# Performance work log

Measured on AMD Instinct MI355X. Metric: run time of the kernel, lower is better.

## Reference

```python
import jax, jax.numpy as jnp
import numpy as np

NEG_SLOPE = 0.2

def gat_conv(x, src, dst, W, a_src, a_dst, b, n_nodes):
    # x: [N, Fin] -> h: [N, Fout]; edges (src->dst) incl. self-loops
    h = x @ W                                   # [N, Fout]
    as_ = h @ a_src                             # [N] per-node source score
    ad_ = h @ a_dst                             # [N] per-node dest score
    e = jax.nn.leaky_relu(as_[src] + ad_[dst], NEG_SLOPE)   # [E]
    # segment softmax over edges sharing the same destination
    e_max = jax.ops.segment_max(e, dst, num_segments=n_nodes)
    e_exp = jnp.exp(e - e_max[dst])
    e_sum = jax.ops.segment_sum(e_exp, dst, num_segments=n_nodes)
    alpha = e_exp / (e_sum[dst] + 1e-16)        # [E]
    out = jax.ops.segment_sum(alpha[:, None] * h[src], dst, num_segments=n_nodes)
    return out + b

def setup_inputs() -> dict:
    key = jax.random.key(0)
    ks = jax.random.split(key, 12)
    N, E, Fin, H = 100000, 3200000, 128, 32
    def g(k, shape, scale):
        return jax.random.normal(k, shape, dtype=jnp.float32) * scale
    return {
        "x": g(ks[0], (N, Fin), 1.0),
        "edge_index": jax.random.randint(ks[1], (2, E), 0, N, dtype=jnp.int32),
        "W1": g(ks[2], (Fin, H), 1.0 / np.sqrt(Fin)),
        "att_src1": g(ks[3], (H,), 1.0 / np.sqrt(H)),
        "att_dst1": g(ks[4], (H,), 1.0 / np.sqrt(H)),
        "b1": jnp.zeros((H,), jnp.float32),
        "W2": g(ks[5], (H, H), 1.0 / np.sqrt(H)),
        "att_src2": g(ks[6], (H,), 1.0 / np.sqrt(H)),
        "att_dst2": g(ks[7], (H,), 1.0 / np.sqrt(H)),
        "b2": jnp.zeros((H,), jnp.float32),
        "Wf": g(ks[8], (H, H), 1.0 / np.sqrt(H)),
        "bf": jnp.zeros((H,), jnp.float32),
    }

def reference(x, edge_index, W1, att_src1, att_dst1, b1, W2, att_src2, att_dst2, b2, Wf, bf):
    n_nodes = x.shape[0]
    loops = jnp.arange(n_nodes, dtype=edge_index.dtype)
    src = jnp.concatenate([edge_index[0], loops])  # add_self_loops=True (PyG default)
    dst = jnp.concatenate([edge_index[1], loops])
    h = jax.nn.relu(gat_conv(x, src, dst, W1, att_src1, att_dst1, b1, n_nodes))
    h = jax.nn.relu(gat_conv(h, src, dst, W2, att_src2, att_dst2, b2, n_nodes))
    return h @ Wf + bf
```

## Files before the change

### kernel.cpp

```cpp
#include <hip/hip_runtime.h>

#define NEG_SLOPE 0.2f
#define BK_SH 8
#define BK_SZ 256
#define MAXBUCK 512
#define EPB 8192

typedef _Float16 half8 __attribute__((ext_vector_type(8)));
typedef float f32x4 __attribute__((ext_vector_type(4)));

__global__ __launch_bounds__(256) void k_castW(const float* __restrict__ W,
                                               _Float16* __restrict__ Wt,
                                               int K) {
  for (int i = threadIdx.x; i < K * 32; i += 256) {
    int k = i >> 5, f = i & 31;
    Wt[f * K + k] = (_Float16)W[i];
  }
}

__global__ __launch_bounds__(256) void k_feat1(
    const float* __restrict__ x, const _Float16* __restrict__ Wt,
    const float* __restrict__ a_src, const float* __restrict__ a_dst,
    _Float16* __restrict__ Hh, float* __restrict__ as_, float* __restrict__ ad_,
    int N) {
  int w = threadIdx.x >> 6;
  int lane = threadIdx.x & 63;
  int base = (blockIdx.x * 4 + w) * 16;
  if (base >= N) return;
  int row16 = lane & 15;
  int kg = lane >> 4;
  f32x4 acc0 = {0.f, 0.f, 0.f, 0.f};
  f32x4 acc1 = {0.f, 0.f, 0.f, 0.f};
  const float* xr = x + (size_t)(base + row16) * 128 + kg * 8;
#pragma unroll
  for (int kt = 0; kt < 4; ++kt) {
    float4 u0 = *reinterpret_cast<const float4*>(xr + kt * 32);
    float4 u1 = *reinterpret_cast<const float4*>(xr + kt * 32 + 4);
    half8 a;
    a[0] = (_Float16)u0.x; a[1] = (_Float16)u0.y;
    a[2] = (_Float16)u0.z; a[3] = (_Float16)u0.w;
    a[4] = (_Float16)u1.x; a[5] = (_Float16)u1.y;
    a[6] = (_Float16)u1.z; a[7] = (_Float16)u1.w;
    half8 b0 = *reinterpret_cast<const half8*>(Wt + (size_t)row16 * 128 +
                                               kt * 32 + kg * 8);
    half8 b1 = *reinterpret_cast<const half8*>(Wt + (size_t)(16 + row16) * 128 +
                                               kt * 32 + kg * 8);
    acc0 = __builtin_amdgcn_mfma_f32_16x16x32_f16(a, b0, acc0, 0, 0, 0);
    acc1 = __builtin_amdgcn_mfma_f32_16x16x32_f16(a, b1, acc1, 0, 0, 0);
  }
  float aS0 = a_src[row16], aS1 = a_src[16 + row16];
  float aD0 = a_dst[row16], aD1 = a_dst[16 + row16];
  float tS[4], tD[4];
#pragma unroll
  for (int r = 0; r < 4; ++r) {
    int row = base + kg * 4 + r;
    Hh[(size_t)row * 32 + row16] = (_Float16)acc0[r];
    Hh[(size_t)row * 32 + 16 + row16] = (_Float16)acc1[r];
    tS[r] = acc0[r] * aS0 + acc1[r] * aS1;
    tD[r] = acc0[r] * aD0 + acc1[r] * aD1;
  }
#pragma unroll
  for (int off = 1; off <= 8; off <<= 1) {
#pragma unroll
    for (int r = 0; r < 4; ++r) {
      tS[r] += __shfl_xor(tS[r], off, 64);
      tD[r] += __shfl_xor(tD[r], off, 64);
    }
  }
  if (row16 == 0) {
#pragma unroll
    for (int r = 0; r < 4; ++r) {
      as_[base + kg * 4 + r] = tS[r];
      ad_[base + kg * 4 + r] = tD[r];
    }
  }
}

__global__ __launch_bounds__(256) void k_feat2(
    const _Float16* __restrict__ Bh, const _Float16* __restrict__ Wt,
    const float* __restrict__ a_src, const float* __restrict__ a_dst,
    _Float16* __restrict__ Hh, float* __restrict__ as_, float* __restrict__ ad_,
    int N) {
  int w = threadIdx.x >> 6;
  int lane = threadIdx.x & 63;
  int base = (blockIdx.x * 4 + w) * 16;
  if (base >= N) return;
  int row16 = lane & 15;
  int kg = lane >> 4;
  half8 a = *reinterpret_cast<const half8*>(Bh + (size_t)(base + row16) * 32 +
                                            kg * 8);
  half8 b0 =
      *reinterpret_cast<const half8*>(Wt + (size_t)row16 * 32 + kg * 8);
  half8 b1 =
      *reinterpret_cast<const half8*>(Wt + (size_t)(16 + row16) * 32 + kg * 8);
  f32x4 acc0 = {0.f, 0.f, 0.f, 0.f};
  f32x4 acc1 = {0.f, 0.f, 0.f, 0.f};
  acc0 = __builtin_amdgcn_mfma_f32_16x16x32_f16(a, b0, acc0, 0, 0, 0);
  acc1 = __builtin_amdgcn_mfma_f32_16x16x32_f16(a, b1, acc1, 0, 0, 0);
  float aS0 = a_src[row16], aS1 = a_src[16 + row16];
  float aD0 = a_dst[row16], aD1 = a_dst[16 + row16];
  float tS[4], tD[4];
#pragma unroll
  for (int r = 0; r < 4; ++r) {
    int row = base + kg * 4 + r;
    Hh[(size_t)row * 32 + row16] = (_Float16)acc0[r];
    Hh[(size_t)row * 32 + 16 + row16] = (_Float16)acc1[r];
    tS[r] = acc0[r] * aS0 + acc1[r] * aS1;
    tD[r] = acc0[r] * aD0 + acc1[r] * aD1;
  }
#pragma unroll
  for (int off = 1; off <= 8; off <<= 1) {
#pragma unroll
    for (int r = 0; r < 4; ++r) {
      tS[r] += __shfl_xor(tS[r], off, 64);
      tD[r] += __shfl_xor(tD[r], off, 64);
    }
  }
  if (row16 == 0) {
#pragma unroll
    for (int r = 0; r < 4; ++r) {
      as_[base + kg * 4 + r] = tS[r];
      ad_[base + kg * 4 + r] = tD[r];
    }
  }
}

__global__ __launch_bounds__(256) void k_zero(int* __restrict__ p, int n) {
  int i = blockIdx.x * 256 + threadIdx.x;
  if (i < n) p[i] = 0;
}

__global__ __launch_bounds__(256) void k_bhist(const int* __restrict__ ei,
                                               int E, int* __restrict__ bcnt,
                                               int* __restrict__ hmatT,
                                               int nb, int nbuck) {
  __shared__ int h[MAXBUCK];
  for (int i = threadIdx.x; i < nbuck; i += 256) h[i] = 0;
  __syncthreads();
  long base = (long)blockIdx.x * EPB;
#pragma unroll 4
  for (int i = 0; i < EPB / 256; ++i) {
    long e = base + i * 256 + threadIdx.x;
    if (e < E) atomicAdd(&h[ei[E + e] >> BK_SH], 1);
  }
  __syncthreads();
  for (int i = threadIdx.x; i < nbuck; i += 256) {
    hmatT[(size_t)i * nb + blockIdx.x] = h[i];
    if (h[i]) atomicAdd(&bcnt[i], h[i]);
  }
}

__global__ __launch_bounds__(1024) void k_scan(const int* __restrict__ bcnt,
                                               int* __restrict__ boff,
                                               int* __restrict__ ptr, int nbuck,
                                               int N, int E) {
  __shared__ int s[1024];
  int t = threadIdx.x;
  int v = (t < nbuck) ? bcnt[t] : 0;
  s[t] = v;
  __syncthreads();
  for (int off = 1; off < 1024; off <<= 1) {
    int x = (t >= off) ? s[t - off] : 0;
    __syncthreads();
    s[t] += x;
    __syncthreads();
  }
  if (t < nbuck) boff[t] = s[t] - v;
  if (t == 0) {
    boff[nbuck] = E;
    ptr[N] = E;
  }
}

__global__ __launch_bounds__(256) void k_colscan(const int* __restrict__ hmatT,
                                                 int* __restrict__ lbgT,
                                                 const int* __restrict__ boff,
                                                 int nb, int nbuck) {
  int wid = (blockIdx.x * 256 + threadIdx.x) >> 6;
  int lane = threadIdx.x & 63;
  if (wid >= nbuck) return;
  const int* row = hmatT + (size_t)wid * nb;
  int* orow = lbgT + (size_t)wid * nb;
  int base = boff[wid];
  for (int c = 0; c < nb; c += 64) {
    int v = (c + lane < nb) ? row[c + lane] : 0;
    int s = v;
#pragma unroll
    for (int off = 1; off < 64; off <<= 1) {
      int x = __shfl_up(s, off, 64);
      if (lane >= off) s += x;
    }
    if (c + lane < nb) orow[c + lane] = base + s - v;
    base += __shfl(s, 63, 64);
  }
}

__global__ __launch_bounds__(256) void k_binA(
    const int* __restrict__ ei, int E, const int* __restrict__ hmatT,
    const int* __restrict__ lbgT, unsigned* __restrict__ packed, int nb,
    int nbuck) {
  __shared__ int h[MAXBUCK];
  __shared__ int lbase[MAXBUCK];
  __shared__ int lb[MAXBUCK];
  __shared__ int cur[MAXBUCK];
  __shared__ int psum[256];
  __shared__ unsigned rec[EPB];
  __shared__ unsigned char bkt[EPB];
  int t = threadIdx.x;
  for (int i = t; i < MAXBUCK; i += 256) {
    h[i] = (i < nbuck) ? hmatT[(size_t)i * nb + blockIdx.x] : 0;
    lbase[i] = (i < nbuck) ? lbgT[(size_t)i * nb + blockIdx.x] : 0;
  }
  __syncthreads();
  long base = (long)blockIdx.x * EPB;
  int cnt = (int)((E - base) < EPB ? (E - base) : EPB);
  int a0 = h[2 * t], a1 = h[2 * t + 1];
  psum[t] = a0 + a1;
  __syncthreads();
  for (int off = 1; off < 256; off <<= 1) {
    int x = (t >= off) ? psum[t - off] : 0;
    __syncthreads();
    psum[t] += x;
    __syncthreads();
  }
  int pex = psum[t] - (a0 + a1);
  lb[2 * t] = pex;
  lb[2 * t + 1] = pex + a0;
  cur[2 * t] = pex;
  cur[2 * t + 1] = pex + a0;
  __syncthreads();
#pragma unroll 4
  for (int i = 0; i < EPB / 256; ++i) {
    int e = i * 256 + t;
    if (e < cnt) {
      int s = ei[base + e], d = ei[E + base + e];
      int b = d >> BK_SH;
      int pos = atomicAdd(&cur[b], 1);
      rec[pos] = ((unsigned)s << 8) | (unsigned)(d & (BK_SZ - 1));
      bkt[pos] = (unsigned char)b;
    }
  }
  __syncthreads();
  for (int i = t; i < cnt; i += 256) {
    int b0 = bkt[i];
    int b = (i >= lb[b0] && i < cur[b0]) ? b0 : b0 + 256;
    packed[(size_t)lbase[b] + (i - lb[b])] = rec[i];
  }
}

__global__ __launch_bounds__(256) void k_binB(const unsigned* __restrict__ packed,
                                              const int* __restrict__ boff,
                                              int* __restrict__ ptr,
                                              int* __restrict__ srcs, int N) {
  int b = blockIdx.x;
  int beg = boff[b], end = boff[b + 1];
  int t = threadIdx.x;
  __shared__ int lcnt[BK_SZ];
  __shared__ int sc[BK_SZ];
  __shared__ int lcur[BK_SZ];
  lcnt[t] = 0;
  __syncthreads();
  for (int i = beg + t; i < end; i += 256)
    atomicAdd(&lcnt[packed[i] & (BK_SZ - 1)], 1);
  __syncthreads();
  int v = lcnt[t];
  sc[t] = v;
  __syncthreads();
  for (int off = 1; off < 256; off <<= 1) {
    int x = (t >= off) ? sc[t - off] : 0;
    __syncthreads();
    sc[t] += x;
    __syncthreads();
  }
  int excl = sc[t] - v;
  int node = (b << BK_SH) + t;
  if (node < N) ptr[node] = beg + excl;
  lcur[t] = excl;
  __syncthreads();
  for (int i = beg + t; i < end; i += 256) {
    unsigned p = packed[i];
    int slot = atomicAdd(&lcur[p & (BK_SZ - 1)], 1);
    srcs[(size_t)beg + slot] = (int)(p >> 8);
  }
}

template <int FINAL>
__global__ __launch_bounds__(256) void k_gatherT(
    const int* __restrict__ ptr, const int* __restrict__ srcs,
    const _Float16* __restrict__ Hh, const float* __restrict__ as_,
    const float* __restrict__ ad_, const float* __restrict__ b,
    const float* __restrict__ Wf, const float* __restrict__ bf,
    void* __restrict__ OUTv, int N) {
  __shared__ float sWf[32 * 32];
  __shared__ float sO[8][33];
  if (FINAL) {
    for (int i = threadIdx.x; i < 32 * 32; i += 256) sWf[i] = Wf[i];
  }
  int g = threadIdx.x >> 5;
  int lane = threadIdx.x & 31;
  int sub = lane >> 2;
  int q = lane & 3;
  int d = blockIdx.x * 8 + g;
  int dc = d < N ? d : N - 1;
  float ad_d = ad_[dc];
  float acc[8] = {0.f, 0.f, 0.f, 0.f, 0.f, 0.f, 0.f, 0.f};
  float sumw = 0.f;
  int beg = ptr[dc], end = ptr[dc + 1];
  bool v0 = sub < end - beg;
  int sid0 = v0 ? srcs[beg + sub] : dc;
  float sa0 = as_[sid0];
  half8 hv0 = *reinterpret_cast<const half8*>(Hh + (size_t)sid0 * 32 + q * 8);
  bool v1 = sub < end - (beg + 8);
  int sid1 = v1 ? srcs[beg + 8 + sub] : dc;
  float sa1 = as_[sid1];
  half8 hv1 = *reinterpret_cast<const half8*>(Hh + (size_t)sid1 * 32 + q * 8);
  int nb8 = (end - beg + 7) >> 3;
  int j = beg;
#pragma unroll 2
  for (int it = 0; it < nb8; ++it) {
    int jn = j + 16;
    bool v2 = sub < end - jn;
    int sid2 = v2 ? srcs[jn + sub] : dc;
    float sa2 = as_[sid2];
    half8 hv2 = *reinterpret_cast<const half8*>(Hh + (size_t)sid2 * 32 + q * 8);
    float sc2 = sa0 + ad_d;
    float el = sc2 > 0.f ? sc2 : NEG_SLOPE * sc2;
    float w = v0 ? __expf(el) : 0.f;
#pragma unroll
    for (int i = 0; i < 8; ++i) acc[i] += w * (float)hv0[i];
    sumw += w;
    j = j + 8;
    v0 = v1; sid0 = sid1; sa0 = sa1; hv0 = hv1;
    v1 = v2; sid1 = sid2; sa1 = sa2; hv1 = hv2;
  }
#pragma unroll
  for (int off = 4; off <= 16; off <<= 1) {
#pragma unroll
    for (int i = 0; i < 8; ++i) acc[i] += __shfl_xor(acc[i], off, 32);
    sumw += __shfl_xor(sumw, off, 32);
  }
  if (sub == 0) {
    float s0 = as_[dc] + ad_d;
    float e0 = s0 > 0.f ? s0 : NEG_SLOPE * s0;
    float w0 = __expf(e0);
    half8 hs = *reinterpret_cast<const half8*>(Hh + (size_t)dc * 32 + q * 8);
#pragma unroll
    for (int i = 0; i < 8; ++i) acc[i] += w0 * (float)hs[i];
    sumw += w0;
    float inv = 1.f / (sumw + 1e-16f);
    if (FINAL) {
#pragma unroll
      for (int i = 0; i < 8; ++i)
        sO[g][q * 8 + i] = fmaxf(acc[i] * inv + b[q * 8 + i], 0.f);
    } else if (d < N) {
      half8 o;
#pragma unroll
      for (int i = 0; i < 8; ++i)
        o[i] = (_Float16)fmaxf(acc[i] * inv + b[q * 8 + i], 0.f);
      *reinterpret_cast<half8*>((_Float16*)OUTv + (size_t)d * 32 + q * 8) = o;
    }
  }
  if (FINAL) {
    __syncthreads();
    float accf = bf[lane];
#pragma unroll
    for (int k = 0; k < 32; ++k) accf += sO[g][k] * sWf[k * 32 + lane];
    if (d < N) ((float*)OUTv)[(size_t)d * 32 + lane] = accf;
  }
}

extern "C" void kernel_launch(void* const* d_in, const int* in_sizes, int n_in,
                              void* d_out, int out_size, void* d_ws,
                              size_t ws_size, hipStream_t stream) {
  const float* x = (const float*)d_in[0];
  const int* ei = (const int*)d_in[1];
  const float* W1 = (const float*)d_in[2];
  const float* as1 = (const float*)d_in[3];
  const float* ad1 = (const float*)d_in[4];
  const float* b1 = (const float*)d_in[5];
  const float* W2 = (const float*)d_in[6];
  const float* as2 = (const float*)d_in[7];
  const float* ad2 = (const float*)d_in[8];
  const float* b2 = (const float*)d_in[9];
  const float* Wf = (const float*)d_in[10];
  const float* bf = (const float*)d_in[11];
  float* out = (float*)d_out;

  const int H = in_sizes[3];
  const int FIN = in_sizes[2] / H;
  const int N = in_sizes[0] / FIN;
  const int E = in_sizes[1] / 2;
  const int nbuck = (N + BK_SZ - 1) >> BK_SH;
  (void)n_in; (void)out_size; (void)ws_size; (void)H;

  const int nodeBlocks = (N + 7) / 8;
  const int binBlocks = (E + EPB - 1) / EPB;
  const int mfmaBlocks = (N / 16 + 3) / 4;

  size_t r0 = (size_t)E * 4;
  size_t bhB = (size_t)N * 32 * 2;
  if (bhB > r0) r0 = bhB;
  char* basep = (char*)d_ws;
  unsigned* packed = (unsigned*)basep;
  _Float16* Bh = (_Float16*)basep;
  char* p = basep + r0;
  _Float16* Hh = (_Float16*)p;   p += (size_t)N * 32 * 2;
  _Float16* Wt1 = (_Float16*)p;  p += (size_t)128 * 32 * 2;
  _Float16* Wt2 = (_Float16*)p;  p += (size_t)32 * 32 * 2;
  float* asv = (float*)p;        p += (size_t)N * 4;
  float* adv = (float*)p;        p += (size_t)N * 4;
  int* ptr = (int*)p;            p += (size_t)(N + 1) * 4;
  int* srcs = (int*)p;           p += (size_t)E * 4;
  int* bcnt = (int*)p;           p += (size_t)nbuck * 4;
  int* boff = (int*)p;           p += (size_t)(nbuck + 1) * 4;
  int* hmatT = (int*)p;          p += (size_t)binBlocks * nbuck * 4;
  int* lbgT = (int*)p;

  k_zero<<<(nbuck + 255) / 256, 256, 0, stream>>>(bcnt, nbuck);
  k_bhist<<<binBlocks, 256, 0, stream>>>(ei, E, bcnt, hmatT, binBlocks, nbuck);
  k_scan<<<1, 1024, 0, stream>>>(bcnt, boff, ptr, nbuck, N, E);
  k_colscan<<<(nbuck * 64 + 255) / 256, 256, 0, stream>>>(hmatT, lbgT, boff,
                                                          binBlocks, nbuck);
  k_binA<<<binBlocks, 256, 0, stream>>>(ei, E, hmatT, lbgT, packed, binBlocks,
                                        nbuck);
  k_binB<<<nbuck, 256, 0, stream>>>(packed, boff, ptr, srcs, N);

  k_castW<<<1, 256, 0, stream>>>(W1, Wt1, 128);
  k_castW<<<1, 256, 0, stream>>>(W2, Wt2, 32);

  k_feat1<<<mfmaBlocks, 256, 0, stream>>>(x, Wt1, as1, ad1, Hh, asv, adv, N);
  k_gatherT<0><<<nodeBlocks, 256, 0, stream>>>(ptr, srcs, Hh, asv, adv, b1,
                                               nullptr, nullptr, Bh, N);

  k_feat2<<<mfmaBlocks, 256, 0, stream>>>(Bh, Wt2, as2, ad2, Hh, asv, adv, N);
  k_gatherT<1><<<nodeBlocks, 256, 0, stream>>>(ptr, srcs, Hh, asv, adv, b2, Wf,
                                               bf, out, N);
}
```

Measured before the change: 218.1 us.

## Fuse layer-2 projection into layer-1 gather and pre-pack source scores with indices

The layer-2 feature transform (W2 matmul plus attention score dots) is folded into the epilogue of the layer-1 gather kernel using a shared-memory 32x32 matvec, so k_feat2 and the intermediate Bh buffer go away. A new k_fill pass writes an int2 record per edge holding the source id and its source score. The gather then does one 8-byte load per edge instead of a dependent index load followed by a random as_ load. The trade-off is two extra full-edge passes that write 8 bytes per edge each, plus fp32 FMA work in place of MFMA for layer 2.

```diff
diff --git a/kernel.cpp b/kernel.cpp
--- a/kernel.cpp
+++ b/kernel.cpp
@@ -48,55 +48,6 @@
     acc0 = __builtin_amdgcn_mfma_f32_16x16x32_f16(a, b0, acc0, 0, 0, 0);
     acc1 = __builtin_amdgcn_mfma_f32_16x16x32_f16(a, b1, acc1, 0, 0, 0);
   }
-  float aS0 = a_src[row16], aS1 = a_src[16 + row16];
-  float aD0 = a_dst[row16], aD1 = a_dst[16 + row16];
-  float tS[4], tD[4];
-#pragma unroll
-  for (int r = 0; r < 4; ++r) {
-    int row = base + kg * 4 + r;
-    Hh[(size_t)row * 32 + row16] = (_Float16)acc0[r];
-    Hh[(size_t)row * 32 + 16 + row16] = (_Float16)acc1[r];
-    tS[r] = acc0[r] * aS0 + acc1[r] * aS1;
-    tD[r] = acc0[r] * aD0 + acc1[r] * aD1;
-  }
-#pragma unroll
-  for (int off = 1; off <= 8; off <<= 1) {
-#pragma unroll
-    for (int r = 0; r < 4; ++r) {
-      tS[r] += __shfl_xor(tS[r], off, 64);
-      tD[r] += __shfl_xor(tD[r], off, 64);
-    }
-  }
-  if (row16 == 0) {
-#pragma unroll
-    for (int r = 0; r < 4; ++r) {
-      as_[base + kg * 4 + r] = tS[r];
-      ad_[base + kg * 4 + r] = tD[r];
-    }
-  }
-}
-
-__global__ __launch_bounds__(256) void k_feat2(
-    const _Float16* __restrict__ Bh, const _Float16* __restrict__ Wt,
-    const float* __restrict__ a_src, const float* __restrict__ a_dst,
-    _Float16* __restrict__ Hh, float* __restrict__ as_, float* __restrict__ ad_,
-    int N) {
-  int w = threadIdx.x >> 6;
-  int lane = threadIdx.x & 63;
-  int base = (blockIdx.x * 4 + w) * 16;
-  if (base >= N) return;
-  int row16 = lane & 15;
-  int kg = lane >> 4;
-  half8 a = *reinterpret_cast<const half8*>(Bh + (size_t)(base + row16) * 32 +
-                                            kg * 8);
-  half8 b0 =
-      *reinterpret_cast<const half8*>(Wt + (size_t)row16 * 32 + kg * 8);
-  half8 b1 =
-      *reinterpret_cast<const half8*>(Wt + (size_t)(16 + row16) * 32 + kg * 8);
-  f32x4 acc0 = {0.f, 0.f, 0.f, 0.f};
-  f32x4 acc1 = {0.f, 0.f, 0.f, 0.f};
-  acc0 = __builtin_amdgcn_mfma_f32_16x16x32_f16(a, b0, acc0, 0, 0, 0);
-  acc1 = __builtin_amdgcn_mfma_f32_16x16x32_f16(a, b1, acc1, 0, 0, 0);
   float aS0 = a_src[row16], aS1 = a_src[16 + row16];
   float aD0 = a_dst[row16], aD1 = a_dst[16 + row16];
   float tS[4], tD[4];
@@ -284,18 +235,32 @@
   }
 }
 
-template <int FINAL>
+__global__ __launch_bounds__(256) void k_fill(const int* __restrict__ srcs,
+                                              const float* __restrict__ as_,
+                                              int2* __restrict__ rec, int E) {
+  int i = blockIdx.x * 256 + threadIdx.x;
+  int stride = gridDim.x * 256;
+  for (int e = i; e < E; e += stride) {
+    int s = srcs[e];
+    int2 r;
+    r.x = s;
+    r.y = __float_as_int(as_[s]);
+    rec[e] = r;
+  }
+}
+
+template <int MODE>
 __global__ __launch_bounds__(256) void k_gatherT(
-    const int* __restrict__ ptr, const int* __restrict__ srcs,
+    const int* __restrict__ ptr, const int2* __restrict__ rec,
     const _Float16* __restrict__ Hh, const float* __restrict__ as_,
     const float* __restrict__ ad_, const float* __restrict__ b,
-    const float* __restrict__ Wf, const float* __restrict__ bf,
-    void* __restrict__ OUTv, int N) {
-  __shared__ float sWf[32 * 32];
+    const float* __restrict__ Wx, const float* __restrict__ aS2p,
+    const float* __restrict__ aD2p, const float* __restrict__ bfp,
+    _Float16* __restrict__ Hh2, float* __restrict__ as2v,
+    float* __restrict__ ad2v, float* __restrict__ OUT, int N) {
+  __shared__ float sW[32 * 32];
   __shared__ float sO[8][33];
-  if (FINAL) {
-    for (int i = threadIdx.x; i < 32 * 32; i += 256) sWf[i] = Wf[i];
-  }
+  for (int i = threadIdx.x; i < 32 * 32; i += 256) sW[i] = Wx[i];
   int g = threadIdx.x >> 5;
   int lane = threadIdx.x & 31;
   int sub = lane >> 2;
@@ -307,31 +272,28 @@
   float sumw = 0.f;
   int beg = ptr[dc], end = ptr[dc + 1];
   bool v0 = sub < end - beg;
-  int sid0 = v0 ? srcs[beg + sub] : dc;
-  float sa0 = as_[sid0];
-  half8 hv0 = *reinterpret_cast<const half8*>(Hh + (size_t)sid0 * 32 + q * 8);
+  int2 r0 = v0 ? rec[beg + sub] : make_int2(dc, 0);
+  half8 hv0 = *reinterpret_cast<const half8*>(Hh + (size_t)r0.x * 32 + q * 8);
   bool v1 = sub < end - (beg + 8);
-  int sid1 = v1 ? srcs[beg + 8 + sub] : dc;
-  float sa1 = as_[sid1];
-  half8 hv1 = *reinterpret_cast<const half8*>(Hh + (size_t)sid1 * 32 + q * 8);
+  int2 r1 = v1 ? rec[beg + 8 + sub] : make_int2(dc, 0);
+  half8 hv1 = *reinterpret_cast<const half8*>(Hh + (size_t)r1.x * 32 + q * 8);
   int nb8 = (end - beg + 7) >> 3;
   int j = beg;
 #pragma unroll 2
   for (int it = 0; it < nb8; ++it) {
     int jn = j + 16;
     bool v2 = sub < end - jn;
-    int sid2 = v2 ? srcs[jn + sub] : dc;
-    float sa2 = as_[sid2];
-    half8 hv2 = *reinterpret_cast<const half8*>(Hh + (size_t)sid2 * 32 + q * 8);
-    float sc2 = sa0 + ad_d;
+    int2 r2 = v2 ? rec[jn + sub] : make_int2(dc, 0);
+    half8 hv2 = *reinterpret_cast<const half8*>(Hh + (size_t)r2.x * 32 + q * 8);
+    float sc2 = __int_as_float(r0.y) + ad_d;
     float el = sc2 > 0.f ? sc2 : NEG_SLOPE * sc2;
     float w = v0 ? __expf(el) : 0.f;
 #pragma unroll
     for (int i = 0; i < 8; ++i) acc[i] += w * (float)hv0[i];
     sumw += w;
-    j = j + 8;
-    v0 = v1; sid0 = sid1; sa0 = sa1; hv0 = hv1;
-    v1 = v2; sid1 = sid2; sa1 = sa2; hv1 = hv2;
+    j = jn - 8;
+    v0 = v1; r0 = r1; hv0 = hv1;
+    v1 = v2; r1 = r2; hv1 = hv2;
   }
 #pragma unroll
   for (int off = 4; off <= 16; off <<= 1) {
@@ -348,24 +310,29 @@
     for (int i = 0; i < 8; ++i) acc[i] += w0 * (float)hs[i];
     sumw += w0;
     float inv = 1.f / (sumw + 1e-16f);
-    if (FINAL) {
-#pragma unroll
-      for (int i = 0; i < 8; ++i)
-        sO[g][q * 8 + i] = fmaxf(acc[i] * inv + b[q * 8 + i], 0.f);
-    } else if (d < N) {
-      half8 o;
-#pragma unroll
-      for (int i = 0; i < 8; ++i)
-        o[i] = (_Float16)fmaxf(acc[i] * inv + b[q * 8 + i], 0.f);
-      *reinterpret_cast<half8*>((_Float16*)OUTv + (size_t)d * 32 + q * 8) = o;
-    }
-  }
-  if (FINAL) {
-    __syncthreads();
-    float accf = bf[lane];
-#pragma unroll
-    for (int k = 0; k < 32; ++k) accf += sO[g][k] * sWf[k * 32 + lane];
-    if (d < N) ((float*)OUTv)[(size_t)d * 32 + lane] = accf;
+#pragma unroll
+    for (int i = 0; i < 8; ++i)
+      sO[g][q * 8 + i] = fmaxf(acc[i] * inv + b[q * 8 + i], 0.f);
+  }
+  __syncthreads();
+  float accf = (MODE == 1) ? bfp[lane] : 0.f;
+#pragma unroll
+  for (int k = 0; k < 32; ++k) accf += sO[g][k] * sW[k * 32 + lane];
+  if (MODE == 1) {
+    if (d < N) OUT[(size_t)d * 32 + lane] = accf;
+  } else {
+    if (d < N) Hh2[(size_t)d * 32 + lane] = (_Float16)accf;
+    float vs = accf * aS2p[lane];
+    float vd = accf * aD2p[lane];
+#pragma unroll
+    for (int off = 1; off < 32; off <<= 1) {
+      vs += __shfl_xor(vs, off, 32);
+      vd += __shfl_xor(vd, off, 32);
+    }
+    if (lane == 0 && d < N) {
+      as2v[d] = vs;
+      ad2v[d] = vd;
+    }
   }
 }
 
@@ -397,18 +364,18 @@
   const int binBlocks = (E + EPB - 1) / EPB;
   const int mfmaBlocks = (N / 16 + 3) / 4;
 
-  size_t r0 = (size_t)E * 4;
-  size_t bhB = (size_t)N * 32 * 2;
-  if (bhB > r0) r0 = bhB;
+  size_t r0 = (size_t)E * 8;
   char* basep = (char*)d_ws;
   unsigned* packed = (unsigned*)basep;
-  _Float16* Bh = (_Float16*)basep;
+  int2* recb = (int2*)basep;
   char* p = basep + r0;
-  _Float16* Hh = (_Float16*)p;   p += (size_t)N * 32 * 2;
+  _Float16* Hh1 = (_Float16*)p;  p += (size_t)N * 32 * 2;
+  _Float16* Hh2 = (_Float16*)p;  p += (size_t)N * 32 * 2;
   _Float16* Wt1 = (_Float16*)p;  p += (size_t)128 * 32 * 2;
-  _Float16* Wt2 = (_Float16*)p;  p += (size_t)32 * 32 * 2;
   float* asv = (float*)p;        p += (size_t)N * 4;
   float* adv = (float*)p;        p += (size_t)N * 4;
+  float* asv2 = (float*)p;       p += (size_t)N * 4;
+  float* adv2 = (float*)p;       p += (size_t)N * 4;
   int* ptr = (int*)p;            p += (size_t)(N + 1) * 4;
   int* srcs = (int*)p;           p += (size_t)E * 4;
   int* bcnt = (int*)p;           p += (size_t)nbuck * 4;
@@ -426,13 +393,16 @@
   k_binB<<<nbuck, 256, 0, stream>>>(packed, boff, ptr, srcs, N);
 
   k_castW<<<1, 256, 0, stream>>>(W1, Wt1, 128);
-  k_castW<<<1, 256, 0, stream>>>(W2, Wt2, 32);
-
-  k_feat1<<<mfmaBlocks, 256, 0, stream>>>(x, Wt1, as1, ad1, Hh, asv, adv, N);
-  k_gatherT<0><<<nodeBlocks, 256, 0, stream>>>(ptr, srcs, Hh, asv, adv, b1,
-                                               nullptr, nullptr, Bh, N);
-
-  k_feat2<<<mfmaBlocks, 256, 0, stream>>>(Bh, Wt2, as2, ad2, Hh, asv, adv, N);
-  k_gatherT<1><<<nodeBlocks, 256, 0, stream>>>(ptr, srcs, Hh, asv, adv, b2, Wf,
-                                               bf, out, N);
-}
+
+  k_feat1<<<mfmaBlocks, 256, 0, stream>>>(x, Wt1, as1, ad1, Hh1, asv, adv, N);
+  k_fill<<<2048, 256, 0, stream>>>(srcs, asv, recb, E);
+  k_gatherT<0><<<nodeBlocks, 256, 0, stream>>>(ptr, recb, Hh1, asv, adv, b1,
+                                               W2, as2, ad2, nullptr, Hh2,
+                                               asv2, adv2, nullptr, N);
+
+  k_fill<<<2048, 256, 0, stream>>>(srcs, asv2, recb, E);
+  k_gatherT<1><<<nodeBlocks, 256, 0, stream>>>(ptr, recb, Hh2, asv2, adv2, b2,
+                                               Wf, nullptr, nullptr, bf,
+                                               nullptr, nullptr, nullptr, out,
+                                               N);
+}
```

Result: slower. 248.2 us (+13.8%).
